# Kernel tuning notes

Hardware: AMD Instinct MI355X
Metric: run time of the kernel (lower is better)

Reference implementation:

```python
import jax, jax.numpy as jnp
import numpy as np

B, S, E, H, LSRC, V = 16, 128, 256, 512, 128, 32000


def setup_inputs() -> dict:
    key = jax.random.key(0)
    ks = jax.random.split(key, 8)
    return {
        "y_shift": jax.random.randint(ks[0], (B, S), 0, V),
        "embed_table": jax.random.normal(ks[1], (V, E), jnp.float32) * 0.02,
        "W_ih": jax.random.normal(ks[2], (4 * H, E), jnp.float32) * 0.05,
        "W_hh": jax.random.normal(ks[3], (4 * H, H), jnp.float32) * 0.05,
        "b_ih": jnp.zeros((4 * H,), jnp.float32),
        "b_hh": jnp.zeros((4 * H,), jnp.float32),
        "fused_enc": jax.random.normal(ks[4], (B, LSRC, H), jnp.float32),
        "src_mask": jnp.ones((B, LSRC), jnp.bool_),
        "W_out": jax.random.normal(ks[5], (V, H + H), jnp.float32) * 0.02,
        "b_out": jnp.zeros((V,), jnp.float32),
    }


def reference(y_shift, embed_table, W_ih, W_hh, b_ih, b_hh, fused_enc, src_mask, W_out, b_out):
    emb = embed_table[y_shift]                       # [B, S, E]
    h0 = jnp.zeros((emb.shape[0], H), emb.dtype)
    c0 = jnp.zeros((emb.shape[0], H), emb.dtype)

    def step(carry, x_t):
        h, c = carry
        gates = x_t @ W_ih.T + b_ih + h @ W_hh.T + b_hh   # [B, 4H]
        i, f, g, o = jnp.split(gates, 4, axis=-1)          # torch gate order
        c = jax.nn.sigmoid(f) * c + jax.nn.sigmoid(i) * jnp.tanh(g)
        h = jax.nn.sigmoid(o) * jnp.tanh(c)
        return (h, c), h

    _, hs = jax.lax.scan(step, (h0, c0), emb.transpose(1, 0, 2))  # [S, B, H]
    dec_out = hs.transpose(1, 0, 2)                               # [B, S, H]

    # scaled dot-product attention: queries=dec_out, keys=values=fused_enc
    scores = jnp.einsum("bsh,blh->bsl", dec_out, fused_enc) / jnp.sqrt(jnp.float32(H))
    scores = jnp.where(src_mask[:, None, :], scores, jnp.float32(-1e9))
    probs = jax.nn.softmax(scores, axis=-1)
    context = jnp.einsum("bsl,blh->bsh", probs, fused_enc)        # [B, S, H]

    out_cat = jnp.concatenate([dec_out, context], axis=-1)       # [B, S, 2H]
    logits = out_cat @ W_out.T + b_out                           # [B, S, V]
    return logits
```

## Files before the change

### kernel.cpp

```cpp
#include <hip/hip_runtime.h>
#include <hip/hip_bf16.h>
#include <cstdint>

#define B_   16
#define S_   128
#define E_   256
#define H_   512
#define L_   128
#define V_   32000
#define M_   (B_*S_)
#define G4H  (4*H_)
#define K2H  (2*H_)

typedef _Float16 f16;
typedef _Float16 f16x2 __attribute__((ext_vector_type(2)));
typedef _Float16 f16x4v __attribute__((ext_vector_type(4)));
typedef _Float16 f16x8 __attribute__((ext_vector_type(8)));
typedef float f32x4 __attribute__((ext_vector_type(4)));


__global__ void cast_f16_kernel(const float* __restrict__ src, f16* __restrict__ dst, int n4) {
  int i = blockIdx.x * blockDim.x + threadIdx.x;
  int stride = gridDim.x * blockDim.x;
  for (; i < n4; i += stride) {
    float4 v = ((const float4*)src)[i];
    f16x4v o = {(f16)v.x, (f16)v.y, (f16)v.z, (f16)v.w};
    ((f16x4v*)dst)[i] = o;
  }
}

__global__ void cast_whh_kernel(const float* __restrict__ W, f16* __restrict__ dst) {
  int i = blockIdx.x * blockDim.x + threadIdx.x;
  if (i >= 2048 * 128) return;
  int r = i >> 7, c4 = i & 127;
  int q = r >> 9, j = r & 511;
  int g = j >> 5, jp = j & 31;
  int dr = g * 128 + q * 32 + jp;
  float4 v = ((const float4*)W)[(size_t)r * 128 + c4];
  f16x4v o = {(f16)v.x, (f16)v.y, (f16)v.z, (f16)v.w};
  ((f16x4v*)dst)[(size_t)dr * 128 + c4] = o;
}

__global__ void embed_kernel(const int* __restrict__ y, const float* __restrict__ tbl,
                             f16* __restrict__ emb) {
  int m = blockIdx.x;
  int t = threadIdx.x;
  int idx = y[m];
  float4 v = ((const float4*)(tbl + (size_t)idx * E_))[t];
  f16x4v o = {(f16)v.x, (f16)v.y, (f16)v.z, (f16)v.w};
  ((f16x4v*)(emb + (size_t)m * E_))[t] = o;
}

__global__ void prep_misc_kernel(const float* __restrict__ b_ih, const float* __restrict__ b_hh,
                                 float* __restrict__ bsum, unsigned int* __restrict__ flags) {
  int i = blockIdx.x * blockDim.x + threadIdx.x;
  if (i < G4H) bsum[i] = b_ih[i] + b_hh[i];
  if (i < B_ * 16) flags[i] = 0u;
}

#define BM 128
#define BN 128
#define BK 32

__global__ __launch_bounds__(256) void gemm_f16_kernel(
    const f16* __restrict__ A, const f16* __restrict__ Bm,
    const float* __restrict__ bias, float* __restrict__ C,
    int Mdim, int Ndim, int Kdim) {
  __shared__ __align__(16) f16 As[BM * BK];
  __shared__ __align__(16) f16 Bs[BN * BK];
  int tid = threadIdx.x;
  int wave = tid >> 6, lane = tid & 63;
  int wm = wave >> 1, wn = wave & 1;
  int brow = blockIdx.y * BM, bcol = blockIdx.x * BN;
  f32x4 acc[4][4] = {};
  int fr = lane & 15;
  int ko = (lane >> 4) * 8;

  for (int k0 = 0; k0 < Kdim; k0 += BK) {
#pragma unroll
    for (int j = 0; j < 2; ++j) {
      int chunk = wave * 128 + j * 64 + lane;
      int row = chunk >> 2, seg = chunk & 3;
      const f16* ga = A + (size_t)(brow + row) * Kdim + k0 + seg * 8;
      const f16* gb = Bm + (size_t)(bcol + row) * Kdim + k0 + seg * 8;
      __builtin_amdgcn_global_load_lds(
          (const __attribute__((address_space(1))) void*)ga,
          (__attribute__((address_space(3))) void*)&As[(wave * 128 + j * 64) * 8], 16, 0, 0);
      __builtin_amdgcn_global_load_lds(
          (const __attribute__((address_space(1))) void*)gb,
          (__attribute__((address_space(3))) void*)&Bs[(wave * 128 + j * 64) * 8], 16, 0, 0);
    }
    __syncthreads();
    f16x8 af[4], bf[4];
#pragma unroll
    for (int mt = 0; mt < 4; ++mt)
      af[mt] = *(const f16x8*)&As[(wm * 64 + mt * 16 + fr) * BK + ko];
#pragma unroll
    for (int nt = 0; nt < 4; ++nt)
      bf[nt] = *(const f16x8*)&Bs[(wn * 64 + nt * 16 + fr) * BK + ko];
#pragma unroll
    for (int mt = 0; mt < 4; ++mt)
#pragma unroll
      for (int nt = 0; nt < 4; ++nt)
        acc[mt][nt] = __builtin_amdgcn_mfma_f32_16x16x32_f16(af[mt], bf[nt], acc[mt][nt], 0, 0, 0);
    __syncthreads();
  }
  int cr = (lane >> 4) * 4, cc = lane & 15;
#pragma unroll
  for (int mt = 0; mt < 4; ++mt) {
    int row = brow + wm * 64 + mt * 16 + cr;
#pragma unroll
    for (int nt = 0; nt < 4; ++nt) {
      int col = bcol + wn * 64 + nt * 16 + cc;
      float bv = bias ? bias[col] : 0.f;
#pragma unroll
      for (int r = 0; r < 4; ++r)
        C[(size_t)(row + r) * Ndim + col] = acc[mt][nt][r] + bv;
    }
  }
}

__global__ __launch_bounds__(256) void lstm_kernel(
    const f16* __restrict__ Wsh,
    const float* __restrict__ xW,
    float* __restrict__ dec_out,
    float* __restrict__ h_glob,
    unsigned int* __restrict__ flags)
{
  extern __shared__ char smem[];
  const int STR = 520;
  f16* Wsl = (f16*)smem;
  f16* hb = (f16*)(smem + 128 * STR * 2);
  float* scr = (float*)(smem + 128 * STR * 2 + 1024);
  float* cl = scr + 128;
  int blk = blockIdx.x;
  int b = blk >> 4, g = blk & 15;
  int t = threadIdx.x;

  for (int i = t; i < 128 * 64; i += 256) {
    int row = i >> 6, c = i & 63;
    *(f16x8*)&Wsl[row * STR + c * 8] = *(const f16x8*)&Wsh[((size_t)(g * 128 + row)) * 512 + c * 8];
  }
  hb[2 * t] = (f16)0.f;
  hb[2 * t + 1] = (f16)0.f;
  if (t < 32) cl[t] = 0.f;
  __syncthreads();

  int sr = t >> 1, half = t & 1;
  const f16* wrow = &Wsl[sr * STR + half * 256];
  const f16* hrow = &hb[half * 256];
  unsigned int* fl = flags + b * 16;

  for (int s = 0; s < S_; ++s) {
    float xi = 0.f, xf = 0.f, xg = 0.f, xo = 0.f;
    if (t < 32) {
      const float* xr = xW + (size_t)(b * S_ + s) * G4H + g * 32 + t;
      xi = xr[0]; xf = xr[512]; xg = xr[1024]; xo = xr[1536];
    }

    float acc = 0.f;
#pragma unroll
    for (int i = 0; i < 32; ++i) {
      f16x8 wv = *(const f16x8*)&wrow[i * 8];
      f16x8 hv = *(const f16x8*)&hrow[i * 8];
#if __has_builtin(__builtin_amdgcn_fdot2)
      const f16x2* w2 = (const f16x2*)&wv;
      const f16x2* h2 = (const f16x2*)&hv;
      acc = __builtin_amdgcn_fdot2(w2[0], h2[0], acc, false);
      acc = __builtin_amdgcn_fdot2(w2[1], h2[1], acc, false);
      acc = __builtin_amdgcn_fdot2(w2[2], h2[2], acc, false);
      acc = __builtin_amdgcn_fdot2(w2[3], h2[3], acc, false);
#else
#pragma unroll
      for (int p = 0; p < 8; ++p) acc += (float)wv[p] * (float)hv[p];
#endif
    }
    float tot = acc + __shfl_xor(acc, 1, 64);
    if (half == 0) scr[sr] = tot;
    __syncthreads();

    float* hg = h_glob + (size_t)((s + 1) & 1) * B_ * H_;
    if (t < 32) {
      float gi = scr[t] + xi;
      float gf = scr[32 + t] + xf;
      float gg = scr[64 + t] + xg;
      float go = scr[96 + t] + xo;
      float c_ = cl[t];
      float sI = 1.f / (1.f + __expf(-gi));
      float sF = 1.f / (1.f + __expf(-gf));
      float sO = 1.f / (1.f + __expf(-go));
      float cn = sF * c_ + sI * tanhf(gg);
      float hn = sO * tanhf(cn);
      cl[t] = cn;
      __hip_atomic_store(&hg[b * H_ + g * 32 + t], hn, __ATOMIC_RELAXED, __HIP_MEMORY_SCOPE_AGENT);
      dec_out[(size_t)(b * S_ + s) * H_ + g * 32 + t] = hn;
    }
    if (t < 64) {
      asm volatile("s_waitcnt vmcnt(0)" ::: "memory");
      if (t == 0)
        __hip_atomic_store(&fl[g], (unsigned)(s + 1), __ATOMIC_RELAXED, __HIP_MEMORY_SCOPE_AGENT);
      for (;;) {
        unsigned v = __hip_atomic_load(&fl[t & 15], __ATOMIC_RELAXED, __HIP_MEMORY_SCOPE_AGENT);
        if (__all(v >= (unsigned)(s + 1))) break;
        __builtin_amdgcn_s_sleep(1);
      }
    }
    __syncthreads();
    asm volatile("" ::: "memory");
    float h0 = __hip_atomic_load(&hg[b * H_ + 2 * t], __ATOMIC_RELAXED, __HIP_MEMORY_SCOPE_AGENT);
    float h1 = __hip_atomic_load(&hg[b * H_ + 2 * t + 1], __ATOMIC_RELAXED, __HIP_MEMORY_SCOPE_AGENT);
    hb[2 * t] = (f16)h0;
    hb[2 * t + 1] = (f16)h1;
    __syncthreads();
  }
}

__global__ __launch_bounds__(128) void attn_kernel(
    const float* __restrict__ dec_out, const float* __restrict__ enc,
    const unsigned char* __restrict__ mask8, f16* __restrict__ cat_h) {
  __shared__ float sc[L_];
  __shared__ float red[4];
  __shared__ float pr[L_];
  int m = blockIdx.x;
  int b = m >> 7;
  int t = threadIdx.x;
  int wv = t >> 6, lane = t & 63;
  const float* qp = dec_out + (size_t)m * H_;
  float q[8];
#pragma unroll
  for (int j = 0; j < 8; ++j) q[j] = qp[lane * 8 + j];
#pragma unroll
  for (int j = 0; j < 4; ++j) cat_h[(size_t)m * K2H + t * 4 + j] = (f16)qp[t * 4 + j];

  const float* eb = enc + (size_t)b * L_ * H_;
  for (int i = 0; i < 64; ++i) {
    int l = wv * 64 + i;
    const float* er = eb + (size_t)l * H_ + lane * 8;
    float a = 0.f;
#pragma unroll
    for (int j = 0; j < 8; ++j) a += q[j] * er[j];
#pragma unroll
    for (int off = 32; off >= 1; off >>= 1) a += __shfl_xor(a, off, 64);
    if (lane == 0) sc[l] = a;
  }
  __syncthreads();

  bool i32mode = ((mask8[1] | mask8[2] | mask8[3]) == 0);
  float x = sc[t] * 0.044194173824159216f;
  unsigned char mk = i32mode ? mask8[(size_t)4 * (b * L_ + t)] : mask8[b * L_ + t];
  if (mk == 0) x = -1e9f;
  float mx = x;
#pragma unroll
  for (int off = 32; off >= 1; off >>= 1) mx = fmaxf(mx, __shfl_xor(mx, off, 64));
  if (lane == 0) red[wv] = mx;
  __syncthreads();
  mx = fmaxf(red[0], red[1]);
  float p = __expf(x - mx);
  float sm = p;
#pragma unroll
  for (int off = 32; off >= 1; off >>= 1) sm += __shfl_xor(sm, off, 64);
  if (lane == 0) red[2 + wv] = sm;
  __syncthreads();
  sm = red[2] + red[3];
  pr[t] = p / sm;
  __syncthreads();

  float c0 = 0.f, c1 = 0.f, c2 = 0.f, c3 = 0.f;
  for (int l = 0; l < L_; ++l) {
    float pl = pr[l];
    const float* er = eb + (size_t)l * H_;
    c0 += pl * er[t];
    c1 += pl * er[t + 128];
    c2 += pl * er[t + 256];
    c3 += pl * er[t + 384];
  }
  f16* cp = cat_h + (size_t)m * K2H + H_;
  cp[t] = (f16)c0;
  cp[t + 128] = (f16)c1;
  cp[t + 256] = (f16)c2;
  cp[t + 384] = (f16)c3;
}

extern "C" void kernel_launch(void* const* d_in, const int* in_sizes, int n_in,
                              void* d_out, int out_size, void* d_ws, size_t ws_size,
                              hipStream_t stream) {
  const int* y_shift = (const int*)d_in[0];
  const float* embed_t = (const float*)d_in[1];
  const float* W_ih = (const float*)d_in[2];
  const float* W_hh = (const float*)d_in[3];
  const float* b_ih = (const float*)d_in[4];
  const float* b_hh = (const float*)d_in[5];
  const float* enc = (const float*)d_in[6];
  const unsigned char* mask8 = (const unsigned char*)d_in[7];
  const float* W_out = (const float*)d_in[8];
  const float* b_out = (const float*)d_in[9];
  float* out = (float*)d_out;

  char* ws = (char*)d_ws;
  size_t off = 0;
  f16* W_out_h = (f16*)(ws + off); off += (size_t)V_ * K2H * 2;
  f16* W_ih_h  = (f16*)(ws + off); off += (size_t)G4H * E_ * 2;
  f16* W_hh_h  = (f16*)(ws + off); off += (size_t)G4H * H_ * 2;
  f16* emb_h   = (f16*)(ws + off); off += (size_t)M_ * E_ * 2;
  float* bsum  = (float*)(ws + off); off += (size_t)G4H * 4;
  float* xW    = (float*)(ws + off); off += (size_t)M_ * G4H * 4;
  float* dec_o = (float*)(ws + off); off += (size_t)M_ * H_ * 4;
  float* h_glob= (float*)(ws + off); off += (size_t)2 * B_ * H_ * 4;
  unsigned int* flags = (unsigned int*)(ws + off); off += (size_t)B_ * 16 * 4;
  f16* cat_h   = (f16*)(ws + off); off += (size_t)M_ * K2H * 2;
  (void)ws_size; (void)in_sizes; (void)n_in; (void)out_size;

  hipLaunchKernelGGL(cast_f16_kernel, dim3(2048), dim3(256), 0, stream, W_out, W_out_h, V_ * K2H / 4);
  hipLaunchKernelGGL(cast_f16_kernel, dim3(512), dim3(256), 0, stream, W_ih, W_ih_h, G4H * E_ / 4);
  hipLaunchKernelGGL(cast_whh_kernel, dim3(1024), dim3(256), 0, stream, W_hh, W_hh_h);
  hipLaunchKernelGGL(embed_kernel, dim3(M_), dim3(64), 0, stream, y_shift, embed_t, emb_h);
  hipLaunchKernelGGL(prep_misc_kernel, dim3(8), dim3(256), 0, stream, b_ih, b_hh, bsum, flags);

  hipLaunchKernelGGL(gemm_f16_kernel, dim3(G4H / BN, M_ / BM), dim3(256), 0, stream,
                     emb_h, W_ih_h, bsum, xW, M_, G4H, E_);

  int lds_bytes = 128 * 520 * 2 + 1024 + 128 * 4 + 32 * 4;
  hipFuncSetAttribute((const void*)lstm_kernel, hipFuncAttributeMaxDynamicSharedMemorySize, lds_bytes);
  hipLaunchKernelGGL(lstm_kernel, dim3(256), dim3(256), lds_bytes, stream,
                     W_hh_h, xW, dec_o, h_glob, flags);

  hipLaunchKernelGGL(attn_kernel, dim3(M_), dim3(128), 0, stream, dec_o, enc, mask8, cat_h);

  hipLaunchKernelGGL(gemm_f16_kernel, dim3(V_ / BN, M_ / BM), dim3(256), 0, stream,
                     cat_h, W_out_h, b_out, out, M_, V_, K2H);
}
```

Baseline: 1.108 ms.

## Keep LSTM weights in registers and sync via packed sequence-tagged packets

The recurrent kernel now holds each thread's W_hh slice in registers instead of LDS, and keeps the cell state in a register. The separate hidden-state store, per-block flag, spin-wait and extra barrier are replaced by 64-bit packets. Each packet carries two f16 hidden values plus the step number, so consumers poll the data directly. Padding dynamic LDS forces one block per CU. This is meant to cut per-step cross-block synchronisation latency in the serial recurrence. The costs are high register pressure and reliance on step tags not colliding with stale workspace contents.

```diff
diff --git a/kernel.cpp b/kernel.cpp
--- a/kernel.cpp
+++ b/kernel.cpp
@@ -52,10 +52,9 @@
 }
 
 __global__ void prep_misc_kernel(const float* __restrict__ b_ih, const float* __restrict__ b_hh,
-                                 float* __restrict__ bsum, unsigned int* __restrict__ flags) {
+                                 float* __restrict__ bsum) {
   int i = blockIdx.x * blockDim.x + threadIdx.x;
   if (i < G4H) bsum[i] = b_ih[i] + b_hh[i];
-  if (i < B_ * 16) flags[i] = 0u;
 }
 
 #define BM 128
@@ -120,36 +119,33 @@
   }
 }
 
-__global__ __launch_bounds__(256) void lstm_kernel(
+__global__ __launch_bounds__(256, 1) void lstm_kernel(
     const f16* __restrict__ Wsh,
     const float* __restrict__ xW,
     float* __restrict__ dec_out,
-    float* __restrict__ h_glob,
-    unsigned int* __restrict__ flags)
+    unsigned long long* __restrict__ pkt)
 {
-  extern __shared__ char smem[];
-  const int STR = 520;
-  f16* Wsl = (f16*)smem;
-  f16* hb = (f16*)(smem + 128 * STR * 2);
-  float* scr = (float*)(smem + 128 * STR * 2 + 1024);
-  float* cl = scr + 128;
+  extern __shared__ char lds_pad[];
+  __shared__ f16 hb[512];
+  __shared__ float scr[128];
+  (void)lds_pad;
   int blk = blockIdx.x;
   int b = blk >> 4, g = blk & 15;
   int t = threadIdx.x;
-
-  for (int i = t; i < 128 * 64; i += 256) {
-    int row = i >> 6, c = i & 63;
-    *(f16x8*)&Wsl[row * STR + c * 8] = *(const f16x8*)&Wsh[((size_t)(g * 128 + row)) * 512 + c * 8];
-  }
+  int sr = t >> 1, half = t & 1;
+
+  const f16* wsrc = Wsh + ((size_t)(g * 128 + sr)) * 512 + half * 256;
+  f16x8 wreg[32];
+#pragma unroll
+  for (int i = 0; i < 32; ++i) wreg[i] = *(const f16x8*)&wsrc[i * 8];
+
   hb[2 * t] = (f16)0.f;
   hb[2 * t + 1] = (f16)0.f;
-  if (t < 32) cl[t] = 0.f;
-  __syncthreads();
-
-  int sr = t >> 1, half = t & 1;
-  const f16* wrow = &Wsl[sr * STR + half * 256];
+  float cell = 0.f;
+  __syncthreads();
+
   const f16* hrow = &hb[half * 256];
-  unsigned int* fl = flags + b * 16;
+  int rd_base = (t >> 4) * 32 + (t & 15) * 2;
 
   for (int s = 0; s < S_; ++s) {
     float xi = 0.f, xf = 0.f, xg = 0.f, xo = 0.f;
@@ -161,56 +157,59 @@
     float acc = 0.f;
 #pragma unroll
     for (int i = 0; i < 32; ++i) {
-      f16x8 wv = *(const f16x8*)&wrow[i * 8];
       f16x8 hv = *(const f16x8*)&hrow[i * 8];
+      const f16x2* w2 = (const f16x2*)&wreg[i];
+      const f16x2* h2 = (const f16x2*)&hv;
 #if __has_builtin(__builtin_amdgcn_fdot2)
-      const f16x2* w2 = (const f16x2*)&wv;
-      const f16x2* h2 = (const f16x2*)&hv;
       acc = __builtin_amdgcn_fdot2(w2[0], h2[0], acc, false);
       acc = __builtin_amdgcn_fdot2(w2[1], h2[1], acc, false);
       acc = __builtin_amdgcn_fdot2(w2[2], h2[2], acc, false);
       acc = __builtin_amdgcn_fdot2(w2[3], h2[3], acc, false);
 #else
 #pragma unroll
-      for (int p = 0; p < 8; ++p) acc += (float)wv[p] * (float)hv[p];
+      for (int p = 0; p < 4; ++p) {
+        acc += (float)w2[p][0] * (float)h2[p][0];
+        acc += (float)w2[p][1] * (float)h2[p][1];
+      }
 #endif
     }
     float tot = acc + __shfl_xor(acc, 1, 64);
     if (half == 0) scr[sr] = tot;
     __syncthreads();
 
-    float* hg = h_glob + (size_t)((s + 1) & 1) * B_ * H_;
+    unsigned long long* pb = pkt + (size_t)((s + 1) & 1) * (B_ * 256) + b * 256;
     if (t < 32) {
       float gi = scr[t] + xi;
       float gf = scr[32 + t] + xf;
       float gg = scr[64 + t] + xg;
       float go = scr[96 + t] + xo;
-      float c_ = cl[t];
       float sI = 1.f / (1.f + __expf(-gi));
       float sF = 1.f / (1.f + __expf(-gf));
       float sO = 1.f / (1.f + __expf(-go));
-      float cn = sF * c_ + sI * tanhf(gg);
+      float cn = sF * cell + sI * tanhf(gg);
       float hn = sO * tanhf(cn);
-      cl[t] = cn;
-      __hip_atomic_store(&hg[b * H_ + g * 32 + t], hn, __ATOMIC_RELAXED, __HIP_MEMORY_SCOPE_AGENT);
+      cell = cn;
       dec_out[(size_t)(b * S_ + s) * H_ + g * 32 + t] = hn;
-    }
-    if (t < 64) {
-      asm volatile("s_waitcnt vmcnt(0)" ::: "memory");
-      if (t == 0)
-        __hip_atomic_store(&fl[g], (unsigned)(s + 1), __ATOMIC_RELAXED, __HIP_MEMORY_SCOPE_AGENT);
-      for (;;) {
-        unsigned v = __hip_atomic_load(&fl[t & 15], __ATOMIC_RELAXED, __HIP_MEMORY_SCOPE_AGENT);
-        if (__all(v >= (unsigned)(s + 1))) break;
-        __builtin_amdgcn_s_sleep(1);
+      float hn_odd = __shfl_xor(hn, 1, 64);
+      if ((t & 1) == 0) {
+        unsigned short ua = __builtin_bit_cast(unsigned short, (f16)hn);
+        unsigned short ub = __builtin_bit_cast(unsigned short, (f16)hn_odd);
+        unsigned long long packet =
+            ((unsigned long long)(unsigned)(s + 1) << 32) |
+            ((unsigned long long)ub << 16) | ua;
+        __hip_atomic_store(&pb[g * 16 + (t >> 1)], packet,
+                           __ATOMIC_RELAXED, __HIP_MEMORY_SCOPE_AGENT);
       }
     }
-    __syncthreads();
-    asm volatile("" ::: "memory");
-    float h0 = __hip_atomic_load(&hg[b * H_ + 2 * t], __ATOMIC_RELAXED, __HIP_MEMORY_SCOPE_AGENT);
-    float h1 = __hip_atomic_load(&hg[b * H_ + 2 * t + 1], __ATOMIC_RELAXED, __HIP_MEMORY_SCOPE_AGENT);
-    hb[2 * t] = (f16)h0;
-    hb[2 * t + 1] = (f16)h1;
+    unsigned long long v;
+    for (;;) {
+      v = __hip_atomic_load(&pb[t], __ATOMIC_RELAXED, __HIP_MEMORY_SCOPE_AGENT);
+      if ((unsigned)(v >> 32) == (unsigned)(s + 1)) break;
+      __builtin_amdgcn_s_sleep(1);
+    }
+    unsigned int d = (unsigned int)v;
+    hb[rd_base]     = __builtin_bit_cast(f16, (unsigned short)(d & 0xffffu));
+    hb[rd_base + 1] = __builtin_bit_cast(f16, (unsigned short)(d >> 16));
     __syncthreads();
   }
 }
@@ -305,8 +304,8 @@
   float* bsum  = (float*)(ws + off); off += (size_t)G4H * 4;
   float* xW    = (float*)(ws + off); off += (size_t)M_ * G4H * 4;
   float* dec_o = (float*)(ws + off); off += (size_t)M_ * H_ * 4;
-  float* h_glob= (float*)(ws + off); off += (size_t)2 * B_ * H_ * 4;
-  unsigned int* flags = (unsigned int*)(ws + off); off += (size_t)B_ * 16 * 4;
+  unsigned long long* pkt = (unsigned long long*)(ws + off);
+  off += (size_t)2 * B_ * 256 * 8;
   f16* cat_h   = (f16*)(ws + off); off += (size_t)M_ * K2H * 2;
   (void)ws_size; (void)in_sizes; (void)n_in; (void)out_size;
 
@@ -314,15 +313,15 @@
   hipLaunchKernelGGL(cast_f16_kernel, dim3(512), dim3(256), 0, stream, W_ih, W_ih_h, G4H * E_ / 4);
   hipLaunchKernelGGL(cast_whh_kernel, dim3(1024), dim3(256), 0, stream, W_hh, W_hh_h);
   hipLaunchKernelGGL(embed_kernel, dim3(M_), dim3(64), 0, stream, y_shift, embed_t, emb_h);
-  hipLaunchKernelGGL(prep_misc_kernel, dim3(8), dim3(256), 0, stream, b_ih, b_hh, bsum, flags);
+  hipLaunchKernelGGL(prep_misc_kernel, dim3(8), dim3(256), 0, stream, b_ih, b_hh, bsum);
 
   hipLaunchKernelGGL(gemm_f16_kernel, dim3(G4H / BN, M_ / BM), dim3(256), 0, stream,
                      emb_h, W_ih_h, bsum, xW, M_, G4H, E_);
 
-  int lds_bytes = 128 * 520 * 2 + 1024 + 128 * 4 + 32 * 4;
+  int lds_bytes = 84 * 1024;
   hipFuncSetAttribute((const void*)lstm_kernel, hipFuncAttributeMaxDynamicSharedMemorySize, lds_bytes);
   hipLaunchKernelGGL(lstm_kernel, dim3(256), dim3(256), lds_bytes, stream,
-                     W_hh_h, xW, dec_o, h_glob, flags);
+                     W_hh_h, xW, dec_o, pkt);
 
   hipLaunchKernelGGL(attn_kernel, dim3(M_), dim3(128), 0, stream, dec_o, enc, mask8, cat_h);
 
```

After: 895.7 us. 1.24x faster.
